# Kernel tuning notes

Measured on AMD Instinct MI355X. Metric: run time of the kernel, lower is better.

## Reference

```python
import jax, jax.numpy as jnp
import numpy as np

DIM = 4096
HID = 11008  # multiple_of*ceil(int(2*(4*dim)/3)/multiple_of)
R = 16
SCALING = 32.0 / 16.0  # lora_alpha / r = 2.0


def setup_inputs() -> dict:
    key = jax.random.key(0)
    ks = jax.random.split(key, 10)
    s_in = 1.0 / np.sqrt(DIM)
    s_hid = 1.0 / np.sqrt(HID)
    return {
        "x": jax.random.normal(ks[0], (4, 2048, DIM), jnp.float32),
        "w1": jax.random.normal(ks[1], (HID, DIM), jnp.float32) * s_in,
        "w3": jax.random.normal(ks[2], (HID, DIM), jnp.float32) * s_in,
        "w2": jax.random.normal(ks[3], (DIM, HID), jnp.float32) * s_hid,
        "lora_A1": jax.random.normal(ks[4], (R, DIM), jnp.float32) * s_in,
        "lora_B1": jax.random.normal(ks[5], (HID, R), jnp.float32) * 0.02,
        "lora_A3": jax.random.normal(ks[6], (R, DIM), jnp.float32) * s_in,
        "lora_B3": jax.random.normal(ks[7], (HID, R), jnp.float32) * 0.02,
        "lora_A2": jax.random.normal(ks[8], (R, HID), jnp.float32) * s_hid,
        "lora_B2": jax.random.normal(ks[9], (DIM, R), jnp.float32) * 0.02,
    }


def _lora_linear(x, w, a, b):
    # result = x @ w.T + ((x @ a.T) @ b.T) * scaling   (no dropout, bias=False)
    base = jnp.einsum("bsd,od->bso", x, w)
    low = jnp.einsum("bsr,or->bso", jnp.einsum("bsd,rd->bsr", x, a), b)
    return base + low * SCALING


def reference(x, w1, w3, w2, lora_A1, lora_B1, lora_A3, lora_B3, lora_A2, lora_B2):
    h1 = _lora_linear(x, w1, lora_A1, lora_B1)  # [B,S,HID]
    h3 = _lora_linear(x, w3, lora_A3, lora_B3)  # [B,S,HID]
    g = jax.nn.silu(h1) * h3                    # SwiGLU gate
    return _lora_linear(g, w2, lora_A2, lora_B2)  # [B,S,DIM]
```

## Files before the change

### kernel.cpp

```cpp
#include <hip/hip_runtime.h>
#include <hip/hip_bf16.h>
#include <cstdint>
#include <cstddef>

typedef _Float16 f16;
typedef _Float16 f16x8 __attribute__((ext_vector_type(8)));
typedef float f32x4 __attribute__((ext_vector_type(4)));

#define DIMK 4096
#define HIDK 11008
#define MTOK 8192

__device__ __forceinline__ void gld_lds16(const void* g, void* l) {
  __builtin_amdgcn_global_load_lds(
      (const __attribute__((address_space(1))) void*)g,
      (__attribute__((address_space(3))) void*)l, 16, 0, 0);
}

__global__ __launch_bounds__(256) void convertk(const float* __restrict__ s,
                                                f16* __restrict__ d, int n) {
  for (int i = ((int)blockIdx.x * 256 + (int)threadIdx.x) * 8; i < n;
       i += (int)gridDim.x * 256 * 8) {
    const float4* p = (const float4*)(s + i);
    float4 a = p[0], b = p[1];
    f16x8 o;
    o[0] = (f16)a.x; o[1] = (f16)a.y; o[2] = (f16)a.z; o[3] = (f16)a.w;
    o[4] = (f16)b.x; o[5] = (f16)b.y; o[6] = (f16)b.z; o[7] = (f16)b.w;
    *(f16x8*)(d + i) = o;
  }
}

__global__ __launch_bounds__(256) void lora_xA(const f16* __restrict__ xh,
                                               const float* __restrict__ A1,
                                               const float* __restrict__ A3,
                                               float* __restrict__ t1,
                                               float* __restrict__ t3) {
  const int wid = threadIdx.x >> 6, l = threadIdx.x & 63;
  const int m = (int)blockIdx.x * 4 + wid;
  float a1[16], a3[16];
#pragma unroll
  for (int r = 0; r < 16; ++r) { a1[r] = 0.f; a3[r] = 0.f; }
  for (int it = 0; it < 8; ++it) {
    const int k0 = it * 512 + l * 8;
    f16x8 xv = *(const f16x8*)(xh + (size_t)m * DIMK + k0);
    float xf[8];
#pragma unroll
    for (int j = 0; j < 8; ++j) xf[j] = (float)xv[j];
#pragma unroll
    for (int r = 0; r < 16; ++r) {
      const float4* p1 = (const float4*)(A1 + (size_t)r * DIMK + k0);
      float4 u = p1[0], v = p1[1];
      a1[r] += xf[0]*u.x + xf[1]*u.y + xf[2]*u.z + xf[3]*u.w +
               xf[4]*v.x + xf[5]*v.y + xf[6]*v.z + xf[7]*v.w;
      const float4* p3 = (const float4*)(A3 + (size_t)r * DIMK + k0);
      float4 s2 = p3[0], t2v = p3[1];
      a3[r] += xf[0]*s2.x + xf[1]*s2.y + xf[2]*s2.z + xf[3]*s2.w +
               xf[4]*t2v.x + xf[5]*t2v.y + xf[6]*t2v.z + xf[7]*t2v.w;
    }
  }
#pragma unroll
  for (int r = 0; r < 16; ++r) {
    float v1 = a1[r], v3 = a3[r];
#pragma unroll
    for (int off = 32; off > 0; off >>= 1) {
      v1 += __shfl_xor(v1, off);
      v3 += __shfl_xor(v3, off);
    }
    if (l == 0) { t1[m * 16 + r] = v1; t3[m * 16 + r] = v3; }
  }
}

__global__ __launch_bounds__(256) void lora_g(const f16* __restrict__ gh,
                                              const float* __restrict__ A2,
                                              float* __restrict__ t2) {
  const int wid = threadIdx.x >> 6, l = threadIdx.x & 63;
  const int m = (int)blockIdx.x * 4 + wid;
  float acc[16];
#pragma unroll
  for (int r = 0; r < 16; ++r) acc[r] = 0.f;
  for (int it = 0; it < 22; ++it) {
    const int k0 = it * 512 + l * 8;
    if (k0 < HIDK) {
      f16x8 gv = *(const f16x8*)(gh + (size_t)m * HIDK + k0);
      float xf[8];
#pragma unroll
      for (int j = 0; j < 8; ++j) xf[j] = (float)gv[j];
#pragma unroll
      for (int r = 0; r < 16; ++r) {
        const float4* p = (const float4*)(A2 + (size_t)r * HIDK + k0);
        float4 u = p[0], v = p[1];
        acc[r] += xf[0]*u.x + xf[1]*u.y + xf[2]*u.z + xf[3]*u.w +
                  xf[4]*v.x + xf[5]*v.y + xf[6]*v.z + xf[7]*v.w;
      }
    }
  }
#pragma unroll
  for (int r = 0; r < 16; ++r) {
    float v = acc[r];
#pragma unroll
    for (int off = 32; off > 0; off >>= 1) v += __shfl_xor(v, off);
    if (l == 0) t2[m * 16 + r] = v;
  }
}

__global__ __launch_bounds__(256, 2) void gemm_gate(
    const f16* __restrict__ xh, const f16* __restrict__ w1h,
    const f16* __restrict__ w3h, const float* __restrict__ t1,
    const float* __restrict__ t3, const float* __restrict__ B1,
    const float* __restrict__ B3, f16* __restrict__ gh) {
  __shared__ __align__(16) char sX[16384];
  __shared__ __align__(16) char sW1[16384];
  __shared__ __align__(16) char sW3[16384];

  const int bid = (int)blockIdx.x;
  const int wg = (bid & 7) * 688 + (bid >> 3);
  const int tm = wg & 63, tn = wg >> 6;
  const int M0 = tm * 128, N0 = tn * 128;

  const int tid = threadIdx.x;
  const int wid = tid >> 6, l = tid & 63;
  const int wr = wid >> 1, wc = wid & 1;

  const f32x4 zz = {0.f, 0.f, 0.f, 0.f};
  f32x4 acc1[4][4], acc3[4][4];
#pragma unroll
  for (int i = 0; i < 4; ++i)
#pragma unroll
    for (int j = 0; j < 4; ++j) { acc1[i][j] = zz; acc3[i][j] = zz; }

  const int rl = l >> 3, cb = (l & 7) << 4;
  const int scb = cb ^ (rl << 4);
  const char* xg = (const char*)xh + ((size_t)(M0 + wid * 32 + rl) << 13) + scb;
  const char* w1g = (const char*)w1h + ((size_t)(N0 + wid * 32 + rl) << 13) + scb;
  const char* w3g = (const char*)w3h + ((size_t)(N0 + wid * 32 + rl) << 13) + scb;
  char* lX = sX + wid * 4096;
  char* lW1 = sW1 + wid * 4096;
  char* lW3 = sW3 + wid * 4096;

  for (int kb = 0; kb < 64; ++kb) {
    const size_t ko = (size_t)kb << 7;
#pragma unroll
    for (int q = 0; q < 4; ++q) {
      gld_lds16(xg + ko + q * 65536, lX + q * 1024);
      gld_lds16(w1g + ko + q * 65536, lW1 + q * 1024);
      gld_lds16(w3g + ko + q * 65536, lW3 + q * 1024);
    }
    asm volatile("s_waitcnt vmcnt(0)" ::: "memory");
    __syncthreads();
#pragma unroll
    for (int ks = 0; ks < 2; ++ks) {
      const int clin = ks * 64 + ((l >> 4) << 4);
      const int sx = (l & 7) << 4;
      f16x8 a[4];
#pragma unroll
      for (int i = 0; i < 4; ++i)
        a[i] = *(const f16x8*)(sX + ((wr * 64 + i * 16 + (l & 15)) << 7) +
                               (clin ^ sx));
#pragma unroll
      for (int j = 0; j < 4; ++j) {
        const int off =
            ((wc * 64 + j * 16 + (l & 15)) << 7) + (clin ^ sx);
        const f16x8 b1 = *(const f16x8*)(sW1 + off);
        const f16x8 b3 = *(const f16x8*)(sW3 + off);
#pragma unroll
        for (int i = 0; i < 4; ++i) {
          acc1[i][j] = __builtin_amdgcn_mfma_f32_16x16x32_f16(a[i], b1, acc1[i][j], 0, 0, 0);
          acc3[i][j] = __builtin_amdgcn_mfma_f32_16x16x32_f16(a[i], b3, acc3[i][j], 0, 0, 0);
        }
      }
    }
    __syncthreads();
  }

  {
    const int row = tid >> 1, h = tid & 1;
    const int s = (row & 7) << 4;
    const int c0 = h << 5;
    const float* sa = h ? (t3 + (size_t)(M0 + row) * 16)
                        : (t1 + (size_t)(M0 + row) * 16);
    f16x8 lo, hi;
#pragma unroll
    for (int r = 0; r < 8; ++r) {
      lo[r] = (f16)(2.0f * sa[r]);
      hi[r] = (f16)(2.0f * sa[r + 8]);
    }
    char* prX = sX + (row << 7);
    *(f16x8*)(prX + (c0 ^ s)) = lo;
    *(f16x8*)(prX + ((c0 + 16) ^ s)) = hi;

    const float* sb1 = B1 + (size_t)(N0 + row) * 16;
    const float* sb3 = B3 + (size_t)(N0 + row) * 16;
    f16x8 v1lo, v1hi, v3lo, v3hi;
#pragma unroll
    for (int r = 0; r < 8; ++r) {
      if (h == 0) {
        v1lo[r] = (f16)sb1[r]; v1hi[r] = (f16)sb1[r + 8];
        v3lo[r] = (f16)0.f;    v3hi[r] = (f16)0.f;
      } else {
        v1lo[r] = (f16)0.f;    v1hi[r] = (f16)0.f;
        v3lo[r] = (f16)sb3[r]; v3hi[r] = (f16)sb3[r + 8];
      }
    }
    char* pr1 = sW1 + (row << 7);
    char* pr3 = sW3 + (row << 7);
    *(f16x8*)(pr1 + (c0 ^ s)) = v1lo;
    *(f16x8*)(pr1 + ((c0 + 16) ^ s)) = v1hi;
    *(f16x8*)(pr3 + (c0 ^ s)) = v3lo;
    *(f16x8*)(pr3 + ((c0 + 16) ^ s)) = v3hi;
  }
  __syncthreads();
  {
    const int clin = (l >> 4) << 4;
    const int sx = (l & 7) << 4;
    f16x8 a[4];
#pragma unroll
    for (int i = 0; i < 4; ++i)
      a[i] = *(const f16x8*)(sX + ((wr * 64 + i * 16 + (l & 15)) << 7) +
                             (clin ^ sx));
#pragma unroll
    for (int j = 0; j < 4; ++j) {
      const int off = ((wc * 64 + j * 16 + (l & 15)) << 7) + (clin ^ sx);
      const f16x8 b1 = *(const f16x8*)(sW1 + off);
      const f16x8 b3 = *(const f16x8*)(sW3 + off);
#pragma unroll
      for (int i = 0; i < 4; ++i) {
        acc1[i][j] = __builtin_amdgcn_mfma_f32_16x16x32_f16(a[i], b1, acc1[i][j], 0, 0, 0);
        acc3[i][j] = __builtin_amdgcn_mfma_f32_16x16x32_f16(a[i], b3, acc3[i][j], 0, 0, 0);
      }
    }
  }

#pragma unroll
  for (int i = 0; i < 4; ++i)
#pragma unroll
    for (int j = 0; j < 4; ++j) {
      const int n = N0 + wc * 64 + j * 16 + (l & 15);
#pragma unroll
      for (int r = 0; r < 4; ++r) {
        const int m = M0 + wr * 64 + i * 16 + ((l >> 4) << 2) + r;
        const float h1 = acc1[i][j][r], h3 = acc3[i][j][r];
        const float gg = h1 * h3 / (1.f + __expf(-h1));
        gh[(size_t)m * HIDK + n] = (f16)gg;
      }
    }
}

__global__ __launch_bounds__(256, 2) void gemm_out(
    const f16* __restrict__ gh, const f16* __restrict__ w2h,
    const float* __restrict__ t2, const float* __restrict__ B2,
    float* __restrict__ out) {
  __shared__ __align__(16) char sG[16384];
  __shared__ __align__(16) char sW[16384];

  const int bid = (int)blockIdx.x;
  const int wg = (bid & 7) * 256 + (bid >> 3);
  const int tm = wg & 63, tn = wg >> 6;
  const int M0 = tm * 128, N0 = tn * 128;

  const int tid = threadIdx.x;
  const int wid = tid >> 6, l = tid & 63;
  const int wr = wid >> 1, wc = wid & 1;

  const f32x4 zz = {0.f, 0.f, 0.f, 0.f};
  f32x4 acc[4][4];
#pragma unroll
  for (int i = 0; i < 4; ++i)
#pragma unroll
    for (int j = 0; j < 4; ++j) acc[i][j] = zz;

  const int rl = l >> 3, cb = (l & 7) << 4;
  const int scb = cb ^ (rl << 4);
  const size_t RS = (size_t)HIDK * 2;
  const char* gg = (const char*)gh + (size_t)(M0 + wid * 32 + rl) * RS + scb;
  const char* wg2 = (const char*)w2h + (size_t)(N0 + wid * 32 + rl) * RS + scb;
  char* lG = sG + wid * 4096;
  char* lW = sW + wid * 4096;

  for (int kb = 0; kb < 172; ++kb) {
    const size_t ko = (size_t)kb << 7;
#pragma unroll
    for (int q = 0; q < 4; ++q) {
      gld_lds16(gg + ko + q * 8 * RS, lG + q * 1024);
      gld_lds16(wg2 + ko + q * 8 * RS, lW + q * 1024);
    }
    asm volatile("s_waitcnt vmcnt(0)" ::: "memory");
    __syncthreads();
#pragma unroll
    for (int ks = 0; ks < 2; ++ks) {
      const int clin = ks * 64 + ((l >> 4) << 4);
      const int sx = (l & 7) << 4;
      f16x8 a[4];
#pragma unroll
      for (int i = 0; i < 4; ++i)
        a[i] = *(const f16x8*)(sG + ((wr * 64 + i * 16 + (l & 15)) << 7) +
                               (clin ^ sx));
#pragma unroll
      for (int j = 0; j < 4; ++j) {
        const int off = ((wc * 64 + j * 16 + (l & 15)) << 7) + (clin ^ sx);
        const f16x8 b = *(const f16x8*)(sW + off);
#pragma unroll
        for (int i = 0; i < 4; ++i)
          acc[i][j] = __builtin_amdgcn_mfma_f32_16x16x32_f16(a[i], b, acc[i][j], 0, 0, 0);
      }
    }
    __syncthreads();
  }

  {
    const int row = tid >> 1, h = tid & 1;
    const int s = (row & 7) << 4;
    const int c0 = h << 5;
    f16x8 alo, ahi, blo, bhi;
    if (h == 0) {
      const float* sa = t2 + (size_t)(M0 + row) * 16;
      const float* sb = B2 + (size_t)(N0 + row) * 16;
#pragma unroll
      for (int r = 0; r < 8; ++r) {
        alo[r] = (f16)(2.0f * sa[r]); ahi[r] = (f16)(2.0f * sa[r + 8]);
        blo[r] = (f16)sb[r];          bhi[r] = (f16)sb[r + 8];
      }
    } else {
#pragma unroll
      for (int r = 0; r < 8; ++r) {
        alo[r] = (f16)0.f; ahi[r] = (f16)0.f;
        blo[r] = (f16)0.f; bhi[r] = (f16)0.f;
      }
    }
    char* prG = sG + (row << 7);
    char* prW = sW + (row << 7);
    *(f16x8*)(prG + (c0 ^ s)) = alo;
    *(f16x8*)(prG + ((c0 + 16) ^ s)) = ahi;
    *(f16x8*)(prW + (c0 ^ s)) = blo;
    *(f16x8*)(prW + ((c0 + 16) ^ s)) = bhi;
  }
  __syncthreads();
  {
    const int clin = (l >> 4) << 4;
    const int sx = (l & 7) << 4;
    f16x8 a[4];
#pragma unroll
    for (int i = 0; i < 4; ++i)
      a[i] = *(const f16x8*)(sG + ((wr * 64 + i * 16 + (l & 15)) << 7) +
                             (clin ^ sx));
#pragma unroll
    for (int j = 0; j < 4; ++j) {
      const int off = ((wc * 64 + j * 16 + (l & 15)) << 7) + (clin ^ sx);
      const f16x8 b = *(const f16x8*)(sW + off);
#pragma unroll
      for (int i = 0; i < 4; ++i)
        acc[i][j] = __builtin_amdgcn_mfma_f32_16x16x32_f16(a[i], b, acc[i][j], 0, 0, 0);
    }
  }

#pragma unroll
  for (int i = 0; i < 4; ++i)
#pragma unroll
    for (int j = 0; j < 4; ++j) {
      const int n = N0 + wc * 64 + j * 16 + (l & 15);
#pragma unroll
      for (int r = 0; r < 4; ++r) {
        const int m = M0 + wr * 64 + i * 16 + ((l >> 4) << 2) + r;
        out[(size_t)m * DIMK + n] = acc[i][j][r];
      }
    }
}

extern "C" void kernel_launch(void* const* d_in, const int* in_sizes, int n_in,
                              void* d_out, int out_size, void* d_ws,
                              size_t ws_size, hipStream_t stream) {
  (void)in_sizes; (void)n_in; (void)out_size; (void)ws_size;
  const float* x = (const float*)d_in[0];
  const float* w1 = (const float*)d_in[1];
  const float* w3 = (const float*)d_in[2];
  const float* w2 = (const float*)d_in[3];
  const float* A1 = (const float*)d_in[4];
  const float* B1 = (const float*)d_in[5];
  const float* A3 = (const float*)d_in[6];
  const float* B3 = (const float*)d_in[7];
  const float* A2 = (const float*)d_in[8];
  const float* B2 = (const float*)d_in[9];
  float* out = (float*)d_out;
  char* ws = (char*)d_ws;

  f16* xh = (f16*)(ws);
  f16* w1h = (f16*)(ws + 67108864);
  f16* w3h = (f16*)(ws + 67108864 + 90177536);
  f16* w2h = (f16*)(ws + 67108864 + 2 * 90177536);
  f16* gh = (f16*)(ws + 67108864 + 3 * 90177536);
  float* t1 = (float*)(ws + 67108864 + 3 * 90177536 + 180355072);
  float* t3 = t1 + MTOK * 16;
  float* t2 = t3 + MTOK * 16;

  convertk<<<1024, 256, 0, stream>>>(x, xh, MTOK * DIMK);
  convertk<<<1024, 256, 0, stream>>>(w1, w1h, HIDK * DIMK);
  convertk<<<1024, 256, 0, stream>>>(w3, w3h, HIDK * DIMK);
  convertk<<<1024, 256, 0, stream>>>(w2, w2h, DIMK * HIDK);
  lora_xA<<<MTOK / 4, 256, 0, stream>>>(xh, A1, A3, t1, t3);
  gemm_gate<<<(MTOK / 128) * (HIDK / 128), 256, 0, stream>>>(xh, w1h, w3h, t1,
                                                             t3, B1, B3, gh);
  lora_g<<<MTOK / 4, 256, 0, stream>>>(gh, A2, t2);
  gemm_out<<<(MTOK / 128) * (DIMK / 128), 256, 0, stream>>>(gh, w2h, t2, B2,
                                                            out);
}
```

Baseline: 3.574 ms.

## Rewrite both GEMMs with 8-wave larger tiles and 4-stage LDS pipeline

Both GEMM kernels move to 512-thread blocks with larger output tiles (256x128 for the gate GEMM, 256x256 for the output GEMM) and a 4-buffer, 3-deep prefetch pipeline using direct global-to-LDS loads over 32-element K steps. Compute is split into two half-phases with barriers, scheduling barriers and wave priority raising so loads overlap MFMA work. The LoRA rank-16 correction is applied directly from registers instead of being staged through LDS. The aim is to hide global memory latency, which the old single-buffered loop exposed, and to raise reuse per loaded byte. In exchange it needs 128 KB of LDS per block and many more accumulator registers, which may limit occupancy.

```diff
diff --git a/kernel.cpp b/kernel.cpp
--- a/kernel.cpp
+++ b/kernel.cpp
@@ -103,263 +103,303 @@
   }
 }
 
-__global__ __launch_bounds__(256, 2) void gemm_gate(
+#define GNT 128
+__global__ __launch_bounds__(512, 2) void gemm_gate(
     const f16* __restrict__ xh, const f16* __restrict__ w1h,
     const f16* __restrict__ w3h, const float* __restrict__ t1,
     const float* __restrict__ t3, const float* __restrict__ B1,
     const float* __restrict__ B3, f16* __restrict__ gh) {
-  __shared__ __align__(16) char sX[16384];
-  __shared__ __align__(16) char sW1[16384];
-  __shared__ __align__(16) char sW3[16384];
+  __shared__ __align__(16) char lds[131072];
 
   const int bid = (int)blockIdx.x;
-  const int wg = (bid & 7) * 688 + (bid >> 3);
-  const int tm = wg & 63, tn = wg >> 6;
-  const int M0 = tm * 128, N0 = tn * 128;
-
-  const int tid = threadIdx.x;
-  const int wid = tid >> 6, l = tid & 63;
-  const int wr = wid >> 1, wc = wid & 1;
+  const int wg = (bid & 7) * 344 + (bid >> 3);
+  const int tm = wg & 31, tn = wg >> 5;
+  const int M0 = tm << 8, N0 = tn << 7;
+
+  const int tid = (int)threadIdx.x;
+  const int l = tid & 63, wid = tid >> 6;
+  const int wr = wid >> 2, wc = wid & 3;
+  const int rA = l & 15;
+
+  const int srow = l >> 2;
+  const int scol = ((l & 3) ^ ((l >> 3) & 3)) << 4;
+  const uint8_t* aSrc =
+      (const uint8_t*)xh + (size_t)(M0 + wid * 32 + srow) * 8192 + scol;
+  const uint8_t* b1Src =
+      (const uint8_t*)w1h + (size_t)(N0 + wid * 16 + srow) * 8192 + scol;
+  const uint8_t* b3Src =
+      (const uint8_t*)w3h + (size_t)(N0 + wid * 16 + srow) * 8192 + scol;
+
+  const int colA = ((l >> 4) ^ ((l >> 1) & 3)) << 4;
+  const int aOff = ((wr * 128 + rA) << 6) + colA;
+  const int bOff = ((wc * 32 + rA) << 6) + colA;
 
   const f32x4 zz = {0.f, 0.f, 0.f, 0.f};
-  f32x4 acc1[4][4], acc3[4][4];
-#pragma unroll
-  for (int i = 0; i < 4; ++i)
-#pragma unroll
-    for (int j = 0; j < 4; ++j) { acc1[i][j] = zz; acc3[i][j] = zz; }
-
-  const int rl = l >> 3, cb = (l & 7) << 4;
-  const int scb = cb ^ (rl << 4);
-  const char* xg = (const char*)xh + ((size_t)(M0 + wid * 32 + rl) << 13) + scb;
-  const char* w1g = (const char*)w1h + ((size_t)(N0 + wid * 32 + rl) << 13) + scb;
-  const char* w3g = (const char*)w3h + ((size_t)(N0 + wid * 32 + rl) << 13) + scb;
-  char* lX = sX + wid * 4096;
-  char* lW1 = sW1 + wid * 4096;
-  char* lW3 = sW3 + wid * 4096;
-
-  for (int kb = 0; kb < 64; ++kb) {
-    const size_t ko = (size_t)kb << 7;
-#pragma unroll
-    for (int q = 0; q < 4; ++q) {
-      gld_lds16(xg + ko + q * 65536, lX + q * 1024);
-      gld_lds16(w1g + ko + q * 65536, lW1 + q * 1024);
-      gld_lds16(w3g + ko + q * 65536, lW3 + q * 1024);
-    }
-    asm volatile("s_waitcnt vmcnt(0)" ::: "memory");
-    __syncthreads();
-#pragma unroll
-    for (int ks = 0; ks < 2; ++ks) {
-      const int clin = ks * 64 + ((l >> 4) << 4);
-      const int sx = (l & 7) << 4;
-      f16x8 a[4];
-#pragma unroll
-      for (int i = 0; i < 4; ++i)
-        a[i] = *(const f16x8*)(sX + ((wr * 64 + i * 16 + (l & 15)) << 7) +
-                               (clin ^ sx));
-#pragma unroll
-      for (int j = 0; j < 4; ++j) {
-        const int off =
-            ((wc * 64 + j * 16 + (l & 15)) << 7) + (clin ^ sx);
-        const f16x8 b1 = *(const f16x8*)(sW1 + off);
-        const f16x8 b3 = *(const f16x8*)(sW3 + off);
-#pragma unroll
-        for (int i = 0; i < 4; ++i) {
-          acc1[i][j] = __builtin_amdgcn_mfma_f32_16x16x32_f16(a[i], b1, acc1[i][j], 0, 0, 0);
-          acc3[i][j] = __builtin_amdgcn_mfma_f32_16x16x32_f16(a[i], b3, acc3[i][j], 0, 0, 0);
-        }
-      }
-    }
-    __syncthreads();
-  }
-
+  f32x4 acc1[8][2], acc3[8][2];
+#pragma unroll
+  for (int i = 0; i < 8; ++i)
+#pragma unroll
+    for (int j = 0; j < 2; ++j) { acc1[i][j] = zz; acc3[i][j] = zz; }
+
+#pragma unroll
+  for (int pt = 0; pt < 3; ++pt) {
+    const int bb = pt << 15;
+    const size_t o = (size_t)pt * 64;
+    gld_lds16(aSrc + o, lds + bb + wid * 2048);
+    gld_lds16(aSrc + o + 131072, lds + bb + wid * 2048 + 1024);
+    gld_lds16(b1Src + o, lds + bb + 16384 + wid * 1024);
+    gld_lds16(b3Src + o, lds + bb + 24576 + wid * 1024);
+  }
+  asm volatile("s_waitcnt vmcnt(8)" ::: "memory");
+  __builtin_amdgcn_s_barrier();
+
+  for (int t = 0; t < GNT; ++t) {
+    const int bb = (t & 3) << 15;
+    f16x8 a[8], b1[2], b3[2];
+#pragma unroll
+    for (int i = 0; i < 4; ++i)
+      a[i] = *(const f16x8*)(lds + bb + aOff + i * 1024);
+#pragma unroll
+    for (int j = 0; j < 2; ++j) {
+      b1[j] = *(const f16x8*)(lds + bb + 16384 + bOff + j * 1024);
+      b3[j] = *(const f16x8*)(lds + bb + 24576 + bOff + j * 1024);
+    }
+    if (t + 3 < GNT) {
+      const int nb = ((t + 3) & 3) << 15;
+      const size_t o = (size_t)(t + 3) * 64;
+      gld_lds16(aSrc + o, lds + nb + wid * 2048);
+      gld_lds16(aSrc + o + 131072, lds + nb + wid * 2048 + 1024);
+    }
+    __builtin_amdgcn_s_barrier();
+    asm volatile("s_waitcnt lgkmcnt(0)" ::: "memory");
+    __builtin_amdgcn_sched_barrier(0);
+    __builtin_amdgcn_s_setprio(1);
+#pragma unroll
+    for (int i = 0; i < 4; ++i)
+#pragma unroll
+      for (int j = 0; j < 2; ++j) {
+        acc1[i][j] = __builtin_amdgcn_mfma_f32_16x16x32_f16(a[i], b1[j], acc1[i][j], 0, 0, 0);
+        acc3[i][j] = __builtin_amdgcn_mfma_f32_16x16x32_f16(a[i], b3[j], acc3[i][j], 0, 0, 0);
+      }
+    __builtin_amdgcn_s_setprio(0);
+    __builtin_amdgcn_s_barrier();
+#pragma unroll
+    for (int i = 4; i < 8; ++i)
+      a[i] = *(const f16x8*)(lds + bb + aOff + i * 1024);
+    if (t + 3 < GNT) {
+      const int nb = ((t + 3) & 3) << 15;
+      const size_t o = (size_t)(t + 3) * 64;
+      gld_lds16(b1Src + o, lds + nb + 16384 + wid * 1024);
+      gld_lds16(b3Src + o, lds + nb + 24576 + wid * 1024);
+    }
+    if (t + 3 < GNT)      asm volatile("s_waitcnt vmcnt(8)" ::: "memory");
+    else if (t + 3 == GNT) asm volatile("s_waitcnt vmcnt(4)" ::: "memory");
+    else if (t + 2 == GNT) asm volatile("s_waitcnt vmcnt(0)" ::: "memory");
+    __builtin_amdgcn_s_barrier();
+    asm volatile("s_waitcnt lgkmcnt(0)" ::: "memory");
+    __builtin_amdgcn_sched_barrier(0);
+    __builtin_amdgcn_s_setprio(1);
+#pragma unroll
+    for (int i = 4; i < 8; ++i)
+#pragma unroll
+      for (int j = 0; j < 2; ++j) {
+        acc1[i][j] = __builtin_amdgcn_mfma_f32_16x16x32_f16(a[i], b1[j], acc1[i][j], 0, 0, 0);
+        acc3[i][j] = __builtin_amdgcn_mfma_f32_16x16x32_f16(a[i], b3[j], acc3[i][j], 0, 0, 0);
+      }
+    __builtin_amdgcn_s_setprio(0);
+    __builtin_amdgcn_s_barrier();
+  }
+
+  const int kg = l >> 4;
   {
-    const int row = tid >> 1, h = tid & 1;
-    const int s = (row & 7) << 4;
-    const int c0 = h << 5;
-    const float* sa = h ? (t3 + (size_t)(M0 + row) * 16)
-                        : (t1 + (size_t)(M0 + row) * 16);
-    f16x8 lo, hi;
-#pragma unroll
-    for (int r = 0; r < 8; ++r) {
-      lo[r] = (f16)(2.0f * sa[r]);
-      hi[r] = (f16)(2.0f * sa[r + 8]);
-    }
-    char* prX = sX + (row << 7);
-    *(f16x8*)(prX + (c0 ^ s)) = lo;
-    *(f16x8*)(prX + ((c0 + 16) ^ s)) = hi;
-
-    const float* sb1 = B1 + (size_t)(N0 + row) * 16;
-    const float* sb3 = B3 + (size_t)(N0 + row) * 16;
-    f16x8 v1lo, v1hi, v3lo, v3hi;
-#pragma unroll
-    for (int r = 0; r < 8; ++r) {
-      if (h == 0) {
-        v1lo[r] = (f16)sb1[r]; v1hi[r] = (f16)sb1[r + 8];
-        v3lo[r] = (f16)0.f;    v3hi[r] = (f16)0.f;
+    f16x8 bx1[2], bx3[2];
+#pragma unroll
+    for (int j = 0; j < 2; ++j) {
+      const int n = N0 + wc * 32 + j * 16 + rA;
+#pragma unroll
+      for (int e = 0; e < 8; ++e) { bx1[j][e] = (f16)0.f; bx3[j][e] = (f16)0.f; }
+      if (kg < 2) {
+        const float4* p = (const float4*)(B1 + (size_t)n * 16 + kg * 8);
+        float4 u = p[0], v = p[1];
+        bx1[j][0]=(f16)u.x; bx1[j][1]=(f16)u.y; bx1[j][2]=(f16)u.z; bx1[j][3]=(f16)u.w;
+        bx1[j][4]=(f16)v.x; bx1[j][5]=(f16)v.y; bx1[j][6]=(f16)v.z; bx1[j][7]=(f16)v.w;
       } else {
-        v1lo[r] = (f16)0.f;    v1hi[r] = (f16)0.f;
-        v3lo[r] = (f16)sb3[r]; v3hi[r] = (f16)sb3[r + 8];
-      }
-    }
-    char* pr1 = sW1 + (row << 7);
-    char* pr3 = sW3 + (row << 7);
-    *(f16x8*)(pr1 + (c0 ^ s)) = v1lo;
-    *(f16x8*)(pr1 + ((c0 + 16) ^ s)) = v1hi;
-    *(f16x8*)(pr3 + (c0 ^ s)) = v3lo;
-    *(f16x8*)(pr3 + ((c0 + 16) ^ s)) = v3hi;
-  }
-  __syncthreads();
-  {
-    const int clin = (l >> 4) << 4;
-    const int sx = (l & 7) << 4;
-    f16x8 a[4];
-#pragma unroll
-    for (int i = 0; i < 4; ++i)
-      a[i] = *(const f16x8*)(sX + ((wr * 64 + i * 16 + (l & 15)) << 7) +
-                             (clin ^ sx));
-#pragma unroll
-    for (int j = 0; j < 4; ++j) {
-      const int off = ((wc * 64 + j * 16 + (l & 15)) << 7) + (clin ^ sx);
-      const f16x8 b1 = *(const f16x8*)(sW1 + off);
-      const f16x8 b3 = *(const f16x8*)(sW3 + off);
-#pragma unroll
-      for (int i = 0; i < 4; ++i) {
-        acc1[i][j] = __builtin_amdgcn_mfma_f32_16x16x32_f16(a[i], b1, acc1[i][j], 0, 0, 0);
-        acc3[i][j] = __builtin_amdgcn_mfma_f32_16x16x32_f16(a[i], b3, acc3[i][j], 0, 0, 0);
-      }
-    }
-  }
-
-#pragma unroll
-  for (int i = 0; i < 4; ++i)
-#pragma unroll
-    for (int j = 0; j < 4; ++j) {
-      const int n = N0 + wc * 64 + j * 16 + (l & 15);
+        const float4* p = (const float4*)(B3 + (size_t)n * 16 + (kg - 2) * 8);
+        float4 u = p[0], v = p[1];
+        bx3[j][0]=(f16)u.x; bx3[j][1]=(f16)u.y; bx3[j][2]=(f16)u.z; bx3[j][3]=(f16)u.w;
+        bx3[j][4]=(f16)v.x; bx3[j][5]=(f16)v.y; bx3[j][6]=(f16)v.z; bx3[j][7]=(f16)v.w;
+      }
+    }
+#pragma unroll
+    for (int i = 0; i < 8; ++i) {
+      const int m = M0 + wr * 128 + i * 16 + rA;
+      const float* src = (kg < 2) ? (t1 + (size_t)m * 16 + kg * 8)
+                                  : (t3 + (size_t)m * 16 + (kg - 2) * 8);
+      const float4* p = (const float4*)src;
+      float4 u = p[0], v = p[1];
+      f16x8 ax;
+      ax[0]=(f16)(2.f*u.x); ax[1]=(f16)(2.f*u.y); ax[2]=(f16)(2.f*u.z); ax[3]=(f16)(2.f*u.w);
+      ax[4]=(f16)(2.f*v.x); ax[5]=(f16)(2.f*v.y); ax[6]=(f16)(2.f*v.z); ax[7]=(f16)(2.f*v.w);
+#pragma unroll
+      for (int j = 0; j < 2; ++j) {
+        acc1[i][j] = __builtin_amdgcn_mfma_f32_16x16x32_f16(ax, bx1[j], acc1[i][j], 0, 0, 0);
+        acc3[i][j] = __builtin_amdgcn_mfma_f32_16x16x32_f16(ax, bx3[j], acc3[i][j], 0, 0, 0);
+      }
+    }
+  }
+
+#pragma unroll
+  for (int i = 0; i < 8; ++i)
+#pragma unroll
+    for (int j = 0; j < 2; ++j) {
+      const int n = N0 + wc * 32 + j * 16 + rA;
 #pragma unroll
       for (int r = 0; r < 4; ++r) {
-        const int m = M0 + wr * 64 + i * 16 + ((l >> 4) << 2) + r;
+        const int m = M0 + wr * 128 + i * 16 + (kg << 2) + r;
         const float h1 = acc1[i][j][r], h3 = acc3[i][j][r];
-        const float gg = h1 * h3 / (1.f + __expf(-h1));
-        gh[(size_t)m * HIDK + n] = (f16)gg;
-      }
-    }
-}
-
-__global__ __launch_bounds__(256, 2) void gemm_out(
+        gh[(size_t)m * HIDK + n] = (f16)(h1 * h3 / (1.f + __expf(-h1)));
+      }
+    }
+}
+
+#define ONT 344
+__global__ __launch_bounds__(512, 2) void gemm_out(
     const f16* __restrict__ gh, const f16* __restrict__ w2h,
     const float* __restrict__ t2, const float* __restrict__ B2,
     float* __restrict__ out) {
-  __shared__ __align__(16) char sG[16384];
-  __shared__ __align__(16) char sW[16384];
+  __shared__ __align__(16) char lds[131072];
 
   const int bid = (int)blockIdx.x;
-  const int wg = (bid & 7) * 256 + (bid >> 3);
-  const int tm = wg & 63, tn = wg >> 6;
-  const int M0 = tm * 128, N0 = tn * 128;
-
-  const int tid = threadIdx.x;
-  const int wid = tid >> 6, l = tid & 63;
-  const int wr = wid >> 1, wc = wid & 1;
+  const int wg = (bid & 7) * 64 + (bid >> 3);
+  const int tm = wg & 31, tn = wg >> 5;
+  const int M0 = tm << 8, N0 = tn << 8;
+
+  const int tid = (int)threadIdx.x;
+  const int l = tid & 63, wid = tid >> 6;
+  const int wr = wid >> 2, wc = wid & 3;
+  const int rA = l & 15;
+
+  const int srow = l >> 2;
+  const int scol = ((l & 3) ^ ((l >> 3) & 3)) << 4;
+  const size_t RS = (size_t)HIDK * 2;
+  const uint8_t* aSrc = (const uint8_t*)gh + (size_t)(M0 + wid * 32 + srow) * RS + scol;
+  const uint8_t* bSrc = (const uint8_t*)w2h + (size_t)(N0 + wid * 32 + srow) * RS + scol;
+
+  const int colA = ((l >> 4) ^ ((l >> 1) & 3)) << 4;
+  const int aOff = ((wr * 128 + rA) << 6) + colA;
+  const int bOff = ((wc * 64 + rA) << 6) + colA;
 
   const f32x4 zz = {0.f, 0.f, 0.f, 0.f};
-  f32x4 acc[4][4];
-#pragma unroll
-  for (int i = 0; i < 4; ++i)
+  f32x4 acc[8][4];
+#pragma unroll
+  for (int i = 0; i < 8; ++i)
 #pragma unroll
     for (int j = 0; j < 4; ++j) acc[i][j] = zz;
 
-  const int rl = l >> 3, cb = (l & 7) << 4;
-  const int scb = cb ^ (rl << 4);
-  const size_t RS = (size_t)HIDK * 2;
-  const char* gg = (const char*)gh + (size_t)(M0 + wid * 32 + rl) * RS + scb;
-  const char* wg2 = (const char*)w2h + (size_t)(N0 + wid * 32 + rl) * RS + scb;
-  char* lG = sG + wid * 4096;
-  char* lW = sW + wid * 4096;
-
-  for (int kb = 0; kb < 172; ++kb) {
-    const size_t ko = (size_t)kb << 7;
-#pragma unroll
-    for (int q = 0; q < 4; ++q) {
-      gld_lds16(gg + ko + q * 8 * RS, lG + q * 1024);
-      gld_lds16(wg2 + ko + q * 8 * RS, lW + q * 1024);
-    }
-    asm volatile("s_waitcnt vmcnt(0)" ::: "memory");
-    __syncthreads();
-#pragma unroll
-    for (int ks = 0; ks < 2; ++ks) {
-      const int clin = ks * 64 + ((l >> 4) << 4);
-      const int sx = (l & 7) << 4;
-      f16x8 a[4];
-#pragma unroll
-      for (int i = 0; i < 4; ++i)
-        a[i] = *(const f16x8*)(sG + ((wr * 64 + i * 16 + (l & 15)) << 7) +
-                               (clin ^ sx));
-#pragma unroll
-      for (int j = 0; j < 4; ++j) {
-        const int off = ((wc * 64 + j * 16 + (l & 15)) << 7) + (clin ^ sx);
-        const f16x8 b = *(const f16x8*)(sW + off);
-#pragma unroll
-        for (int i = 0; i < 4; ++i)
-          acc[i][j] = __builtin_amdgcn_mfma_f32_16x16x32_f16(a[i], b, acc[i][j], 0, 0, 0);
-      }
-    }
-    __syncthreads();
-  }
-
+#pragma unroll
+  for (int pt = 0; pt < 3; ++pt) {
+    const int bb = pt << 15;
+    const size_t o = (size_t)pt * 64;
+    gld_lds16(aSrc + o, lds + bb + wid * 2048);
+    gld_lds16(aSrc + o + 16 * RS, lds + bb + wid * 2048 + 1024);
+    gld_lds16(bSrc + o, lds + bb + 16384 + wid * 2048);
+    gld_lds16(bSrc + o + 16 * RS, lds + bb + 16384 + wid * 2048 + 1024);
+  }
+  asm volatile("s_waitcnt vmcnt(8)" ::: "memory");
+  __builtin_amdgcn_s_barrier();
+
+  for (int t = 0; t < ONT; ++t) {
+    const int bb = (t & 3) << 15;
+    f16x8 a[8], b[4];
+#pragma unroll
+    for (int i = 0; i < 4; ++i)
+      a[i] = *(const f16x8*)(lds + bb + aOff + i * 1024);
+#pragma unroll
+    for (int j = 0; j < 4; ++j)
+      b[j] = *(const f16x8*)(lds + bb + 16384 + bOff + j * 1024);
+    if (t + 3 < ONT) {
+      const int nb = ((t + 3) & 3) << 15;
+      const size_t o = (size_t)(t + 3) * 64;
+      gld_lds16(aSrc + o, lds + nb + wid * 2048);
+      gld_lds16(aSrc + o + 16 * RS, lds + nb + wid * 2048 + 1024);
+    }
+    __builtin_amdgcn_s_barrier();
+    asm volatile("s_waitcnt lgkmcnt(0)" ::: "memory");
+    __builtin_amdgcn_sched_barrier(0);
+    __builtin_amdgcn_s_setprio(1);
+#pragma unroll
+    for (int i = 0; i < 4; ++i)
+#pragma unroll
+      for (int j = 0; j < 4; ++j)
+        acc[i][j] = __builtin_amdgcn_mfma_f32_16x16x32_f16(a[i], b[j], acc[i][j], 0, 0, 0);
+    __builtin_amdgcn_s_setprio(0);
+    __builtin_amdgcn_s_barrier();
+#pragma unroll
+    for (int i = 4; i < 8; ++i)
+      a[i] = *(const f16x8*)(lds + bb + aOff + i * 1024);
+    if (t + 3 < ONT) {
+      const int nb = ((t + 3) & 3) << 15;
+      const size_t o = (size_t)(t + 3) * 64;
+      gld_lds16(bSrc + o, lds + nb + 16384 + wid * 2048);
+      gld_lds16(bSrc + o + 16 * RS, lds + nb + 16384 + wid * 2048 + 1024);
+    }
+    if (t + 3 < ONT)      asm volatile("s_waitcnt vmcnt(8)" ::: "memory");
+    else if (t + 3 == ONT) asm volatile("s_waitcnt vmcnt(4)" ::: "memory");
+    else if (t + 2 == ONT) asm volatile("s_waitcnt vmcnt(0)" ::: "memory");
+    __builtin_amdgcn_s_barrier();
+    asm volatile("s_waitcnt lgkmcnt(0)" ::: "memory");
+    __builtin_amdgcn_sched_barrier(0);
+    __builtin_amdgcn_s_setprio(1);
+#pragma unroll
+    for (int i = 4; i < 8; ++i)
+#pragma unroll
+      for (int j = 0; j < 4; ++j)
+        acc[i][j] = __builtin_amdgcn_mfma_f32_16x16x32_f16(a[i], b[j], acc[i][j], 0, 0, 0);
+    __builtin_amdgcn_s_setprio(0);
+    __builtin_amdgcn_s_barrier();
+  }
+
+  const int kg = l >> 4;
   {
-    const int row = tid >> 1, h = tid & 1;
-    const int s = (row & 7) << 4;
-    const int c0 = h << 5;
-    f16x8 alo, ahi, blo, bhi;
-    if (h == 0) {
-      const float* sa = t2 + (size_t)(M0 + row) * 16;
-      const float* sb = B2 + (size_t)(N0 + row) * 16;
-#pragma unroll
-      for (int r = 0; r < 8; ++r) {
-        alo[r] = (f16)(2.0f * sa[r]); ahi[r] = (f16)(2.0f * sa[r + 8]);
-        blo[r] = (f16)sb[r];          bhi[r] = (f16)sb[r + 8];
-      }
-    } else {
-#pragma unroll
-      for (int r = 0; r < 8; ++r) {
-        alo[r] = (f16)0.f; ahi[r] = (f16)0.f;
-        blo[r] = (f16)0.f; bhi[r] = (f16)0.f;
-      }
-    }
-    char* prG = sG + (row << 7);
-    char* prW = sW + (row << 7);
-    *(f16x8*)(prG + (c0 ^ s)) = alo;
-    *(f16x8*)(prG + ((c0 + 16) ^ s)) = ahi;
-    *(f16x8*)(prW + (c0 ^ s)) = blo;
-    *(f16x8*)(prW + ((c0 + 16) ^ s)) = bhi;
-  }
-  __syncthreads();
-  {
-    const int clin = (l >> 4) << 4;
-    const int sx = (l & 7) << 4;
-    f16x8 a[4];
-#pragma unroll
-    for (int i = 0; i < 4; ++i)
-      a[i] = *(const f16x8*)(sG + ((wr * 64 + i * 16 + (l & 15)) << 7) +
-                             (clin ^ sx));
+    f16x8 bx[4];
 #pragma unroll
     for (int j = 0; j < 4; ++j) {
-      const int off = ((wc * 64 + j * 16 + (l & 15)) << 7) + (clin ^ sx);
-      const f16x8 b = *(const f16x8*)(sW + off);
-#pragma unroll
-      for (int i = 0; i < 4; ++i)
-        acc[i][j] = __builtin_amdgcn_mfma_f32_16x16x32_f16(a[i], b, acc[i][j], 0, 0, 0);
-    }
-  }
-
-#pragma unroll
-  for (int i = 0; i < 4; ++i)
+      const int n = N0 + wc * 64 + j * 16 + rA;
+#pragma unroll
+      for (int e = 0; e < 8; ++e) bx[j][e] = (f16)0.f;
+      if (kg < 2) {
+        const float4* p = (const float4*)(B2 + (size_t)n * 16 + kg * 8);
+        float4 u = p[0], v = p[1];
+        bx[j][0]=(f16)u.x; bx[j][1]=(f16)u.y; bx[j][2]=(f16)u.z; bx[j][3]=(f16)u.w;
+        bx[j][4]=(f16)v.x; bx[j][5]=(f16)v.y; bx[j][6]=(f16)v.z; bx[j][7]=(f16)v.w;
+      }
+    }
+#pragma unroll
+    for (int i = 0; i < 8; ++i) {
+      const int m = M0 + wr * 128 + i * 16 + rA;
+      f16x8 ax;
+#pragma unroll
+      for (int e = 0; e < 8; ++e) ax[e] = (f16)0.f;
+      if (kg < 2) {
+        const float4* p = (const float4*)(t2 + (size_t)m * 16 + kg * 8);
+        float4 u = p[0], v = p[1];
+        ax[0]=(f16)(2.f*u.x); ax[1]=(f16)(2.f*u.y); ax[2]=(f16)(2.f*u.z); ax[3]=(f16)(2.f*u.w);
+        ax[4]=(f16)(2.f*v.x); ax[5]=(f16)(2.f*v.y); ax[6]=(f16)(2.f*v.z); ax[7]=(f16)(2.f*v.w);
+      }
+#pragma unroll
+      for (int j = 0; j < 4; ++j)
+        acc[i][j] = __builtin_amdgcn_mfma_f32_16x16x32_f16(ax, bx[j], acc[i][j], 0, 0, 0);
+    }
+  }
+
+#pragma unroll
+  for (int i = 0; i < 8; ++i)
 #pragma unroll
     for (int j = 0; j < 4; ++j) {
-      const int n = N0 + wc * 64 + j * 16 + (l & 15);
+      const int n = N0 + wc * 64 + j * 16 + rA;
 #pragma unroll
       for (int r = 0; r < 4; ++r) {
-        const int m = M0 + wr * 64 + i * 16 + ((l >> 4) << 2) + r;
+        const int m = M0 + wr * 128 + i * 16 + (kg << 2) + r;
         out[(size_t)m * DIMK + n] = acc[i][j][r];
       }
     }
@@ -396,9 +436,9 @@
   convertk<<<1024, 256, 0, stream>>>(w3, w3h, HIDK * DIMK);
   convertk<<<1024, 256, 0, stream>>>(w2, w2h, DIMK * HIDK);
   lora_xA<<<MTOK / 4, 256, 0, stream>>>(xh, A1, A3, t1, t3);
-  gemm_gate<<<(MTOK / 128) * (HIDK / 128), 256, 0, stream>>>(xh, w1h, w3h, t1,
+  gemm_gate<<<(MTOK / 256) * (HIDK / 128), 512, 0, stream>>>(xh, w1h, w3h, t1,
                                                              t3, B1, B3, gh);
   lora_g<<<MTOK / 4, 256, 0, stream>>>(gh, A2, t2);
-  gemm_out<<<(MTOK / 128) * (DIMK / 128), 256, 0, stream>>>(gh, w2h, t2, B2,
+  gemm_out<<<(MTOK / 256) * (DIMK / 256), 512, 0, stream>>>(gh, w2h, t2, B2,
                                                             out);
 }
```

After: 3.445 ms. -3.6%, faster.
